# Kernel optimization log

Measured on AMD Instinct MI355X. Metric: run time of the kernel, lower is better.

Reference implementation:

```python
import jax, jax.numpy as jnp
import numpy as np

N, E, B_GRAPHS = 50000, 512000, 64
XD, ED, C, H, L = 16, 8, 64, 2, 2
EPS = 1e-5


def setup_inputs() -> dict:
    key = jax.random.key(0)
    ks = jax.random.split(key, 20)
    w = lambda k, shape: jax.random.normal(k, shape, jnp.float32) * 0.1
    return {
        "x": jax.random.normal(ks[0], (N, XD), jnp.float32),
        "edge_attr": jax.random.normal(ks[1], (E, ED), jnp.float32),
        "edge_src": jax.random.randint(ks[2], (E,), 0, N, dtype=jnp.int32),
        "edge_dst": jax.random.randint(ks[3], (E,), 0, N, dtype=jnp.int32),
        "batch": jnp.sort(jax.random.randint(ks[4], (N,), 0, B_GRAPHS, dtype=jnp.int32)),
        "node_W": w(ks[5], (XD, C)), "node_b": jnp.zeros((C,), jnp.float32),
        "edge_W": w(ks[6], (ED, C)), "edge_b": jnp.zeros((C,), jnp.float32),
        "Wq": w(ks[7], (L, C, H * C)), "bq": jnp.zeros((L, H * C), jnp.float32),
        "Wk": w(ks[8], (L, C, H * C)), "bk": jnp.zeros((L, H * C), jnp.float32),
        "Wv": w(ks[9], (L, C, H * C)), "bv": jnp.zeros((L, H * C), jnp.float32),
        "We": w(ks[10], (L, C, H * C)), "be": jnp.zeros((L, H * C), jnp.float32),
        "Wskip": w(ks[11], (L, C, C)), "bskip": jnp.zeros((L, C), jnp.float32),
        "gamma": jnp.ones((L, C), jnp.float32), "beta": jnp.zeros((L, C), jnp.float32),
        "gate_W": w(ks[12], (C, 1)), "gate_b": jnp.zeros((1,), jnp.float32),
        "out_W": w(ks[13], (C, 1)), "out_b": jnp.zeros((1,), jnp.float32),
    }


def reference(x, edge_attr, edge_src, edge_dst, batch,
              node_W, node_b, edge_W, edge_b,
              Wq, bq, Wk, bk, Wv, bv, We, be,
              Wskip, bskip, gamma, beta,
              gate_W, gate_b, out_W, out_b):
    n = x.shape[0]
    h = x @ node_W + node_b                       # node encoder: [N, C]
    e = edge_attr @ edge_W + edge_b               # edge encoder: [E, C]
    scale = 1.0 / jnp.sqrt(jnp.float32(C))
    for i in range(L):
        identity = h
        # TransformerConv (UniMP), concat=False -> mean over heads
        q = (h @ Wq[i] + bq[i]).reshape(n, H, C)
        k = (h @ Wk[i] + bk[i]).reshape(n, H, C)
        v = (h @ Wv[i] + bv[i]).reshape(n, H, C)
        ep = (e @ We[i] + be[i]).reshape(-1, H, C)
        k_e = k[edge_src] + ep                    # [E, H, C]
        v_e = v[edge_src] + ep                    # [E, H, C]
        logits = jnp.einsum('ehc,ehc->eh', q[edge_dst], k_e) * scale
        # segment softmax over incoming edges of each target node
        m = jax.ops.segment_max(logits, edge_dst, num_segments=n)
        a = jnp.exp(logits - m[edge_dst])
        denom = jax.ops.segment_sum(a, edge_dst, num_segments=n)
        alpha = a / denom[edge_dst]               # [E, H]
        agg = jax.ops.segment_sum(alpha[:, :, None] * v_e, edge_dst, num_segments=n)
        out = agg.mean(axis=1) + h @ Wskip[i] + bskip[i]   # root/skip term
        # BatchNorm1d (training mode, biased variance)
        mu = out.mean(axis=0)
        var = out.var(axis=0)
        out = gamma[i] * (out - mu) * jax.lax.rsqrt(var + EPS) + beta[i]
        out = jax.nn.leaky_relu(out, 0.01)
        h = out + identity                        # residual
    # GlobalAttention pooling over graphs
    gate = (h @ gate_W + gate_b)[:, 0]            # [N]
    gm = jax.ops.segment_max(gate, batch, num_segments=B_GRAPHS)
    ge = jnp.exp(gate - gm[batch])
    gd = jax.ops.segment_sum(ge, batch, num_segments=B_GRAPHS)
    wts = ge / gd[batch]
    pooled = jax.ops.segment_sum(wts[:, None] * h, batch, num_segments=B_GRAPHS)
    return jax.nn.sigmoid(pooled @ out_W + out_b)  # [B_GRAPHS, 1]
```

## Files before the change

### kernel.cpp

```cpp
#include <hip/hip_runtime.h>
#include <hip/hip_bf16.h>

typedef unsigned short ushort_t;
typedef __attribute__((ext_vector_type(8))) short short8;
typedef __attribute__((ext_vector_type(4))) float float4v;

__device__ __forceinline__ float bfu_lo(unsigned u) {
    return __uint_as_float(u << 16);
}
__device__ __forceinline__ float bfu_hi(unsigned u) {
    return __uint_as_float(u & 0xffff0000u);
}
__device__ __forceinline__ ushort_t f2bf(float f) {
    __hip_bfloat16 h = __float2bfloat16(f);
    return *reinterpret_cast<ushort_t*>(&h);
}



__global__ __launch_bounds__(256) void setup_kernel(
    const float* __restrict__ x, const float* __restrict__ node_W,
    const float* __restrict__ node_b,
    const float* __restrict__ edge_W, const float* __restrict__ edge_b,
    const float* __restrict__ We, const float* __restrict__ be,
    const float* __restrict__ Wq, const float* __restrict__ bq,
    const float* __restrict__ Wk, const float* __restrict__ bk,
    const float* __restrict__ Wv, const float* __restrict__ bv,
    const float* __restrict__ Wskip, const float* __restrict__ bskip,
    float* __restrict__ h, ushort_t* __restrict__ h_bf,
    int* __restrict__ counts,
    float* __restrict__ Wc, float* __restrict__ bcb,
    ushort_t* __restrict__ Wall_arr, float* __restrict__ Wall_bias,
    ushort_t* __restrict__ wv_arr,
    int O0, int O1, int O2, int N) {
    int b = blockIdx.x, t = threadIdx.x;
    if (b < O0) {
        int idx = b * 256 + t;
        if (idx < N * 64) {
            int n = idx >> 6, c = idx & 63;
            float acc = node_b[c];
#pragma unroll
            for (int j = 0; j < 16; ++j) acc += x[n * 16 + j] * node_W[j * 64 + c];
            h[idx] = acc;
            h_bf[idx] = f2bf(acc);
        }
    } else if (b < O1) {
        int i = (b - O0) * 256 + t;
        if (i < N) counts[i] = 0;
    } else if (b < O2) {
        int tid = (b - O1) * 256 + t;
        if (tid < 2048) {
            int l = tid >> 10, d = (tid >> 7) & 7, j = tid & 127;
            float s = 0.f;
            for (int m = 0; m < 64; ++m) s += edge_W[d * 64 + m] * We[l * 8192 + m * 128 + j];
            Wc[l * 1024 + d * 128 + j] = s;
        } else if (tid < 2048 + 256) {
            int u = tid - 2048;
            int l = u >> 7, j = u & 127;
            float s = be[l * 128 + j];
            for (int m = 0; m < 64; ++m) s += edge_b[m] * We[l * 8192 + m * 128 + j];
            bcb[l * 128 + j] = s;
        }
    } else {
        int tid = (b - O2) * 256 + t;
        if (tid < 2 * 14336) {
            int l = tid / 14336, u = tid % 14336;
            int j = u & 7, ln = (u >> 3) & 63, kch = (u >> 9) & 1, ct = u >> 10;
            int nn = ln & 15, quad = ln >> 4;
            int k = kch * 32 + quad * 8 + j;
            int col = ct * 16 + nn;
            float v = 0.f;
            if (col < 128) {
                int hh = col >> 6, m = col & 63;
                const float* wq = Wq + l * 8192 + k * 128 + hh * 64;
                const float* wk = Wk + l * 8192 + m * 128 + hh * 64;
                float s = 0.f;
                for (int c2 = 0; c2 < 64; ++c2) s += wq[c2] * wk[c2];
                v = 0.125f * s;
            } else if (col < 192) {
                v = Wskip[l * 4096 + k * 64 + (col - 128)];
            }
            Wall_arr[(size_t)l * 14336 + ct * 1024 + kch * 512 + ln * 8 + j] = f2bf(v);
        } else if (tid < 2 * 14336 + 2 * 224) {
            int u = tid - 2 * 14336;
            int l = u / 224, col = u % 224;
            float v = 0.f;
            if (col < 128) {
                int hh = col >> 6, m = col & 63;
                const float* bqp = bq + l * 128 + hh * 64;
                const float* wk = Wk + l * 8192 + m * 128 + hh * 64;
                float s = 0.f;
                for (int c2 = 0; c2 < 64; ++c2) s += bqp[c2] * wk[c2];
                v = 0.125f * s;
            } else if (col < 192) {
                v = bskip[l * 64 + col - 128];
            }
            Wall_bias[l * 224 + col] = v;
        } else if (tid < 2 * 14336 + 2 * 224 + 2 * 8192) {
            int u = tid - (2 * 14336 + 2 * 224);
            int l = u >> 13, r = u & 8191;
            int j = r & 7, ln = (r >> 3) & 63, ct = (r >> 9) & 3, kc = r >> 11;
            int quad = ln >> 4, nn = ln & 15;
            int p = kc * 32 + quad * 8 + j;
            int hh = p >> 6, m = p & 63;
            int c2 = ct * 16 + nn;
            wv_arr[(size_t)l * 8192 + r] = f2bf(Wv[l * 8192 + m * 128 + hh * 64 + c2]);
        }
    }
}

__global__ void combine2_kernel(const float* __restrict__ Wq, const float* __restrict__ bq,
                                const float* __restrict__ bk, const float* __restrict__ bv,
                                const float* __restrict__ Wc, const float* __restrict__ bcb,
                                ushort_t* __restrict__ Wall_arr, float* __restrict__ Wall_bias,
                                float* __restrict__ cst) {
    int tid = blockIdx.x * 256 + threadIdx.x;
    if (tid < 2304) {
        int l = tid / 1152, u = tid % 1152, k = u / 18, j = u % 18;
        float s = 0.f;
        if (j < 16) {
            int hh = j >> 3, d = j & 7;
            for (int c = 0; c < 64; ++c)
                s += Wq[l * 8192 + k * 128 + hh * 64 + c] * Wc[l * 1024 + d * 128 + hh * 64 + c];
        } else {
            int hh = j - 16;
            for (int c = 0; c < 64; ++c)
                s += Wq[l * 8192 + k * 128 + hh * 64 + c] *
                     (bcb[l * 128 + hh * 64 + c] + bk[l * 128 + hh * 64 + c]);
        }
        s *= 0.125f;
        int col = 192 + j;
        int ct = col >> 4, nn = col & 15;
        int kch = k >> 5, quad = (k >> 3) & 3, jj = k & 7;
        int ln = quad * 16 + nn;
        Wall_arr[(size_t)l * 14336 + ct * 1024 + kch * 512 + ln * 8 + jj] = f2bf(s);
    } else if (tid < 2304 + 36) {
        int u = tid - 2304;
        int l = u / 18, j = u % 18;
        float s = 0.f;
        if (j < 16) {
            int hh = j >> 3, d = j & 7;
            for (int c = 0; c < 64; ++c)
                s += bq[l * 128 + hh * 64 + c] * Wc[l * 1024 + d * 128 + hh * 64 + c];
        } else {
            int hh = j - 16;
            for (int c = 0; c < 64; ++c)
                s += bq[l * 128 + hh * 64 + c] *
                     (bcb[l * 128 + hh * 64 + c] + bk[l * 128 + hh * 64 + c]);
        }
        Wall_bias[l * 224 + 192 + j] = 0.125f * s;
    } else if (tid < 2304 + 36 + 128) {
        int u = tid - 2340;
        int l = u >> 6, c = u & 63;
        cst[l * 64 + c] = 0.5f * (bv[l * 128 + c] + bv[l * 128 + 64 + c] +
                                  bcb[l * 128 + c] + bcb[l * 128 + 64 + c]);
    }
}


__global__ void csr_count_kernel(const int* __restrict__ dst, int* __restrict__ counts, int E) {
    int e = blockIdx.x * 256 + threadIdx.x;
    if (e < E) atomicAdd(&counts[dst[e]], 1);
}

__global__ void scan1_kernel(const int* __restrict__ counts, int* __restrict__ rowptr,
                             int* __restrict__ bsums, int N) {
    __shared__ int s[256];
    int t = threadIdx.x, i = blockIdx.x * 256 + t;
    int v = (i < N) ? counts[i] : 0;
    s[t] = v;
    __syncthreads();
    for (int d = 1; d < 256; d <<= 1) {
        int x = (t >= d) ? s[t - d] : 0;
        __syncthreads();
        s[t] += x;
        __syncthreads();
    }
    if (i < N) rowptr[i] = s[t] - v;
    if (t == 255) bsums[blockIdx.x] = s[255];
}

__global__ void scan3_kernel(int* __restrict__ rowptr, const int* __restrict__ bsums,
                             int* __restrict__ cursor, int N, int E, int nb) {
    __shared__ int sh[256];
    int t = threadIdx.x;
    int v = (t < nb) ? bsums[t] : 0;
    sh[t] = v;
    __syncthreads();
    for (int d = 1; d < 256; d <<= 1) {
        int x = (t >= d) ? sh[t - d] : 0;
        __syncthreads();
        sh[t] += x;
        __syncthreads();
    }
    int blk = blockIdx.x;
    int offv = (blk == 0) ? 0 : sh[blk - 1];
    int i = blk * 256 + t;
    if (i < N) {
        int r = rowptr[i] + offv;
        rowptr[i] = r;
        cursor[i] = r;
    }
    if (i == 0) rowptr[N] = E;
}

__global__ void csr_fill_kernel(const int* __restrict__ dst, const int* __restrict__ src,
                                const float* __restrict__ edge_attr, int* __restrict__ cursor,
                                char* __restrict__ erec, int E) {
    int e = blockIdx.x * 256 + threadIdx.x;
    if (e < E) {
        int pos = atomicAdd(&cursor[dst[e]], 1);
        float4 a0 = *(const float4*)(edge_attr + (size_t)e * 8);
        float4 a1 = *(const float4*)(edge_attr + (size_t)e * 8 + 4);
        uint4 w1;
        w1.x = (unsigned)f2bf(a0.x) | ((unsigned)f2bf(a0.y) << 16);
        w1.y = (unsigned)f2bf(a0.z) | ((unsigned)f2bf(a0.w) << 16);
        w1.z = (unsigned)f2bf(a1.x) | ((unsigned)f2bf(a1.y) << 16);
        w1.w = (unsigned)f2bf(a1.z) | ((unsigned)f2bf(a1.w) << 16);
        char* rp = erec + (size_t)pos * 32;
        *(uint4*)rp = make_uint4((unsigned)(src[e] * 128), 0u, 0u, 0u);
        *(uint4*)(rp + 16) = w1;
    }
}


__device__ __forceinline__ void gemm_store(
    int col, float bias, float4v c, int nbase, int N,
    ushort_t* __restrict__ qk2buf, float* __restrict__ outbuf, float* __restrict__ qcbuf) {
    if (col < 128) {
        ushort_t* qp = qk2buf + (size_t)nbase * 128 + col;
#pragma unroll
        for (int r = 0; r < 4; ++r)
            if (nbase + r < N) qp[(size_t)r * 128] = f2bf(c[r] + bias);
    } else if (col < 192) {
        float* op = outbuf + (size_t)nbase * 64 + (col - 128);
#pragma unroll
        for (int r = 0; r < 4; ++r)
            if (nbase + r < N) op[(size_t)r * 64] = c[r] + bias;
    } else if (col < 210) {
        float* qp2 = qcbuf + (size_t)nbase * 20 + (col - 192);
#pragma unroll
        for (int r = 0; r < 4; ++r)
            if (nbase + r < N) qp2[(size_t)r * 20] = c[r] + bias;
    }
}

__global__ __launch_bounds__(256) void qkv_mfma_kernel(
    const ushort_t* __restrict__ h_bf,
    const ushort_t* __restrict__ Wall_arr, const float* __restrict__ Wall_bias,
    ushort_t* __restrict__ qk2buf, float* __restrict__ outbuf, float* __restrict__ qcbuf,
    int N) {
    int wave = threadIdx.x >> 6, lane = threadIdx.x & 63;
    int quad = lane >> 4, nn = lane & 15;
    int n0 = blockIdx.x * 32;
    int nodeA = n0 + nn;       if (nodeA >= N) nodeA = N - 1;
    int nodeB = n0 + 16 + nn;  if (nodeB >= N) nodeB = N - 1;
    const ushort_t* apA = h_bf + (size_t)nodeA * 64 + quad * 8;
    const ushort_t* apB = h_bf + (size_t)nodeB * 64 + quad * 8;
    short8 aA0 = *(const short8*)apA;
    short8 aA1 = *(const short8*)(apA + 32);
    short8 aB0 = *(const short8*)apB;
    short8 aB1 = *(const short8*)(apB + 32);
    int ct_start = (wave < 2) ? wave * 4 : (8 + (wave - 2) * 3);
    int ct_cnt = (wave < 2) ? 4 : 3;
    for (int i = 0; i < ct_cnt; ++i) {
        int ct = ct_start + i;
        const ushort_t* bp = Wall_arr + (size_t)ct * 1024 + lane * 8;
        short8 b0 = *(const short8*)bp;
        short8 b1 = *(const short8*)(bp + 512);
        float4v cA = {0.f, 0.f, 0.f, 0.f};
        float4v cB = {0.f, 0.f, 0.f, 0.f};
        cA = __builtin_amdgcn_mfma_f32_16x16x32_bf16(aA0, b0, cA, 0, 0, 0);
        cA = __builtin_amdgcn_mfma_f32_16x16x32_bf16(aA1, b1, cA, 0, 0, 0);
        cB = __builtin_amdgcn_mfma_f32_16x16x32_bf16(aB0, b0, cB, 0, 0, 0);
        cB = __builtin_amdgcn_mfma_f32_16x16x32_bf16(aB1, b1, cB, 0, 0, 0);
        int col = ct * 16 + nn;
        float bias = Wall_bias[col];
        gemm_store(col, bias, cA, n0 + quad * 4, N, qk2buf, outbuf, qcbuf);
        gemm_store(col, bias, cB, n0 + 16 + quad * 4, N, qk2buf, outbuf, qcbuf);
    }
}


__global__ __launch_bounds__(256) void bnqkv_kernel(
    const float* __restrict__ outbuf_in, const float* __restrict__ bnsums,
    const float* __restrict__ gamma, const float* __restrict__ beta,
    float* __restrict__ h, ushort_t* __restrict__ h_bf,
    const ushort_t* __restrict__ Wall_arr, const float* __restrict__ Wall_bias,
    ushort_t* __restrict__ qk2buf, float* __restrict__ outbuf, float* __restrict__ qcbuf,
    int N) {
    __shared__ ushort_t hb[32 * 64];
    __shared__ float ss_scale[64], ss_shift[64];
    int t = threadIdx.x;
    if (t < 64) {
        float invN = 1.f / (float)N;
        float mean = bnsums[t] * invN;
        float var = bnsums[64 + t] * invN - mean * mean;
        float sc = gamma[t] * rsqrtf(var + 1e-5f);
        ss_scale[t] = sc;
        ss_shift[t] = beta[t] - mean * sc;
    }
    __syncthreads();
    int n0 = blockIdx.x * 32;
    int c = t & 63;
    float sc = ss_scale[c], sh = ss_shift[c];
#pragma unroll
    for (int i = 0; i < 8; ++i) {
        int li = t + i * 256;
        int gidx = n0 * 64 + li;
        float hn = 0.f;
        if (gidx < N * 64) {
            float o = outbuf_in[gidx] * sc + sh;
            o = (o > 0.f) ? o : 0.01f * o;
            hn = h[gidx] + o;
            h[gidx] = hn;
            h_bf[gidx] = f2bf(hn);
        }
        hb[li] = f2bf(hn);
    }
    __syncthreads();
    int wave = t >> 6, lane = t & 63;
    int quad = lane >> 4, nn = lane & 15;
    const ushort_t* apA = hb + nn * 64 + quad * 8;
    const ushort_t* apB = hb + (16 + nn) * 64 + quad * 8;
    short8 aA0 = *(const short8*)apA;
    short8 aA1 = *(const short8*)(apA + 32);
    short8 aB0 = *(const short8*)apB;
    short8 aB1 = *(const short8*)(apB + 32);
    int ct_start = (wave < 2) ? wave * 4 : (8 + (wave - 2) * 3);
    int ct_cnt = (wave < 2) ? 4 : 3;
    for (int i = 0; i < ct_cnt; ++i) {
        int ct = ct_start + i;
        const ushort_t* bp = Wall_arr + (size_t)ct * 1024 + lane * 8;
        short8 b0 = *(const short8*)bp;
        short8 b1 = *(const short8*)(bp + 512);
        float4v cA = {0.f, 0.f, 0.f, 0.f};
        float4v cB = {0.f, 0.f, 0.f, 0.f};
        cA = __builtin_amdgcn_mfma_f32_16x16x32_bf16(aA0, b0, cA, 0, 0, 0);
        cA = __builtin_amdgcn_mfma_f32_16x16x32_bf16(aA1, b1, cA, 0, 0, 0);
        cB = __builtin_amdgcn_mfma_f32_16x16x32_bf16(aB0, b0, cB, 0, 0, 0);
        cB = __builtin_amdgcn_mfma_f32_16x16x32_bf16(aB1, b1, cB, 0, 0, 0);
        int col = ct * 16 + nn;
        float bias = Wall_bias[col];
        gemm_store(col, bias, cA, n0 + quad * 4, N, qk2buf, outbuf, qcbuf);
        gemm_store(col, bias, cB, n0 + 16 + quad * 4, N, qk2buf, outbuf, qcbuf);
    }
}


__global__ __launch_bounds__(256) void attn_kernel(
    const ushort_t* __restrict__ h_bf, const ushort_t* __restrict__ qk2buf,
    const float* __restrict__ qcbuf,
    const char* __restrict__ erec, const int* __restrict__ rowptr,
    ushort_t* __restrict__ haccn, float* __restrict__ sen, float* __restrict__ degw,
    int N) {
    int t = threadIdx.x;
    int lane = t & 63, wid = t >> 6;
    int grp = lane >> 4, l16 = lane & 15;
    int head = l16 >> 3, l8 = l16 & 7;
    const char* hbb = (const char*)h_bf;

    int n = blockIdx.x * 16 + wid * 4 + grp;
    bool active = (n < N);
    int nn = active ? n : (N - 1);
    int start = rowptr[nn];
    int deg = active ? (rowptr[nn + 1] - start) : 0;
    int wdeg = deg;
    wdeg = max(wdeg, __shfl_xor(wdeg, 16));
    wdeg = max(wdeg, __shfl_xor(wdeg, 32));

    float lsum = 0.f;
    float hacc[8] = {0.f, 0.f, 0.f, 0.f, 0.f, 0.f, 0.f, 0.f};
    float se[8]   = {0.f, 0.f, 0.f, 0.f, 0.f, 0.f, 0.f, 0.f};

    if (wdeg > 0) {
        uint4 qr = *(const uint4*)((const char*)qk2buf + (size_t)nn * 256 + head * 128 + l8 * 16);
        float qk0 = bfu_lo(qr.x), qk1 = bfu_hi(qr.x);
        float qk2f = bfu_lo(qr.y), qk3 = bfu_hi(qr.y);
        float qk4 = bfu_lo(qr.z), qk5 = bfu_hi(qr.z);
        float qk6 = bfu_lo(qr.w), qk7 = bfu_hi(qr.w);
        const float* qcp = qcbuf + (size_t)nn * 20;
        float4 qcA = *(const float4*)(qcp + head * 8);
        float4 qcB = *(const float4*)(qcp + head * 8 + 4);
        float qb = qcp[16 + head];

        bool dpos = (deg > 0);
        int dclamp = dpos ? (deg - 1) : 0;

        int offL = *(const int*)(erec + (size_t)(dpos ? (start + min(l16, dclamp)) : 0) * 32);
        int o0 = __shfl(offL, grp * 16);
        uint4 ca = *(const uint4*)(hbb + (size_t)(unsigned)o0 + l8 * 16);
        int gi0 = dpos ? start : 0;
        uint4 ev = *(const uint4*)(erec + (size_t)gi0 * 32 + 16);

        for (int it = 0; it < wdeg; ++it) {
            int itn = it + 1;
            if ((itn & 15) == 0)
                offL = *(const int*)(erec +
                        (size_t)(dpos ? (start + min(itn + l16, dclamp)) : 0) * 32);
            int itc = min(itn, wdeg - 1);
            int on = __shfl(offL, grp * 16 + (itc & 15));
            uint4 na = *(const uint4*)(hbb + (size_t)(unsigned)on + l8 * 16);
            int gin = dpos ? (start + min(itc, dclamp)) : 0;
            uint4 fv = *(const uint4*)(erec + (size_t)gin * 32 + 16);

            float h0 = bfu_lo(ca.x), h1 = bfu_hi(ca.x);
            float h2 = bfu_lo(ca.y), h3 = bfu_hi(ca.y);
            float h4 = bfu_lo(ca.z), h5 = bfu_hi(ca.z);
            float h6 = bfu_lo(ca.w), h7 = bfu_hi(ca.w);
            float dt = qk0 * h0 + qk1 * h1 + qk2f * h2 + qk3 * h3
                     + qk4 * h4 + qk5 * h5 + qk6 * h6 + qk7 * h7;
            dt += __shfl_xor(dt, 1);
            dt += __shfl_xor(dt, 2);
            dt += __shfl_xor(dt, 4);
            float ex0 = bfu_lo(ev.x), ex1 = bfu_hi(ev.x);
            float ex2 = bfu_lo(ev.y), ex3 = bfu_hi(ev.y);
            float ex4 = bfu_lo(ev.z), ex5 = bfu_hi(ev.z);
            float ex6 = bfu_lo(ev.w), ex7 = bfu_hi(ev.w);
            float s0 = dt
                     + qcA.x * ex0 + qcA.y * ex1 + qcA.z * ex2 + qcA.w * ex3
                     + qcB.x * ex4 + qcB.y * ex5 + qcB.z * ex6 + qcB.w * ex7
                     + qb;
            float p = (it < deg) ? __expf(fmaxf(s0, -60.f)) : 0.f;
            lsum += p;
            hacc[0] += p * h0; hacc[1] += p * h1;
            hacc[2] += p * h2; hacc[3] += p * h3;
            hacc[4] += p * h4; hacc[5] += p * h5;
            hacc[6] += p * h6; hacc[7] += p * h7;
            se[0] += p * ex0; se[1] += p * ex1; se[2] += p * ex2; se[3] += p * ex3;
            se[4] += p * ex4; se[5] += p * ex5; se[6] += p * ex6; se[7] += p * ex7;
            ca = na; ev = fv;
        }
    }

    if (active) {
        float inv = (deg > 0) ? (0.5f / lsum) : 0.f;
        unsigned pw0 = (unsigned)f2bf(hacc[0] * inv) | ((unsigned)f2bf(hacc[1] * inv) << 16);
        unsigned pw1 = (unsigned)f2bf(hacc[2] * inv) | ((unsigned)f2bf(hacc[3] * inv) << 16);
        unsigned pw2 = (unsigned)f2bf(hacc[4] * inv) | ((unsigned)f2bf(hacc[5] * inv) << 16);
        unsigned pw3 = (unsigned)f2bf(hacc[6] * inv) | ((unsigned)f2bf(hacc[7] * inv) << 16);
        uint4 pk = make_uint4(pw0, pw1, pw2, pw3);
        *(uint4*)((char*)haccn + (size_t)nn * 256 + head * 128 + l8 * 16) = pk;
        if (l8 == 0) {
            *(float4*)(sen + (size_t)nn * 16 + head * 8) =
                make_float4(se[0] * inv, se[1] * inv, se[2] * inv, se[3] * inv);
            *(float4*)(sen + (size_t)nn * 16 + head * 8 + 4) =
                make_float4(se[4] * inv, se[5] * inv, se[6] * inv, se[7] * inv);
            if (head == 0) degw[nn] = (deg > 0) ? 1.f : 0.f;
        }
    }
}


__global__ __launch_bounds__(256) void vapply_kernel(
    const ushort_t* __restrict__ haccn, const float* __restrict__ sen,
    const float* __restrict__ degw,
    const ushort_t* __restrict__ wv_arr, const float* __restrict__ Wc,
    const float* __restrict__ cst,
    float* __restrict__ outbuf, float* __restrict__ part, int N) {
    __shared__ float Wc_s[1024];
    __shared__ float cst_s[64];
    __shared__ float sen_s[32][16];
    __shared__ float dw_s[32];
    __shared__ float ps[128];
    int t = threadIdx.x;
    for (int i = t; i < 1024; i += 256) Wc_s[i] = Wc[i];
    if (t < 64) cst_s[t] = cst[t];
    int n0 = blockIdx.x * 32;
    for (int i = t; i < 512; i += 256) {
        int ln2 = i >> 4;
        int nc = n0 + ln2; if (nc >= N) nc = N - 1;
        sen_s[ln2][i & 15] = sen[(size_t)nc * 16 + (i & 15)];
    }
    if (t < 32) {
        int nc = n0 + t; if (nc >= N) nc = N - 1;
        dw_s[t] = degw[nc];
    }
    __syncthreads();
    int wave = t >> 6, lane = t & 63;
    int quad = lane >> 4, nn = lane & 15;
    int nodeA = n0 + nn;       if (nodeA >= N) nodeA = N - 1;
    int nodeB = n0 + 16 + nn;  if (nodeB >= N) nodeB = N - 1;
    int ct = wave;
    float4v cA = {0.f, 0.f, 0.f, 0.f};
    float4v cB = {0.f, 0.f, 0.f, 0.f};
#pragma unroll
    for (int kc = 0; kc < 4; ++kc) {
        short8 aA = *(const short8*)(haccn + (size_t)nodeA * 128 + kc * 32 + quad * 8);
        short8 aB = *(const short8*)(haccn + (size_t)nodeB * 128 + kc * 32 + quad * 8);
        short8 bb = *(const short8*)(wv_arr + kc * 2048 + ct * 512 + lane * 8);
        cA = __builtin_amdgcn_mfma_f32_16x16x32_bf16(aA, bb, cA, 0, 0, 0);
        cB = __builtin_amdgcn_mfma_f32_16x16x32_bf16(aB, bb, cB, 0, 0, 0);
    }
    int col = ct * 16 + nn;
    float sa = 0.f, sq = 0.f;
#pragma unroll
    for (int g = 0; g < 2; ++g) {
        float4v acc = g ? cB : cA;
        int lbase = g * 16 + quad * 4;
#pragma unroll
        for (int r = 0; r < 4; ++r) {
            int ln2 = lbase + r;
            int nr = n0 + ln2;
            const float* sp = sen_s[ln2];
            float ep = 0.f;
#pragma unroll
            for (int hh = 0; hh < 2; ++hh)
#pragma unroll
                for (int d = 0; d < 8; ++d)
                    ep += sp[hh * 8 + d] * Wc_s[d * 128 + hh * 64 + col];
            if (nr < N) {
                float val = acc[r] + ep + dw_s[ln2] * cst_s[col] +
                            outbuf[(size_t)nr * 64 + col];
                outbuf[(size_t)nr * 64 + col] = val;
                sa += val;
                sq += val * val;
            }
        }
    }
    sa += __shfl_xor(sa, 16); sa += __shfl_xor(sa, 32);
    sq += __shfl_xor(sq, 16); sq += __shfl_xor(sq, 32);
    if (quad == 0) { ps[col] = sa; ps[64 + col] = sq; }
    __syncthreads();
    if (t < 128) part[(size_t)blockIdx.x * 128 + t] = ps[t];
}


__global__ __launch_bounds__(256) void bnreduce_kernel(const float* __restrict__ part,
                                                       float* __restrict__ bnsums, int nb) {
    int s = blockIdx.x;
    int t = threadIdx.x;
    float a = 0.f;
    for (int b = t; b < nb; b += 256) a += part[(size_t)b * 128 + s];
    __shared__ float sh[256];
    sh[t] = a;
    __syncthreads();
    for (int d = 128; d; d >>= 1) {
        if (t < d) sh[t] += sh[t + d];
        __syncthreads();
    }
    if (t == 0) bnsums[s] = sh[0];
}

__global__ __launch_bounds__(256) void bnapply_kernel(
    const float* __restrict__ outbuf, const float* __restrict__ bnsums,
    const float* __restrict__ gamma, const float* __restrict__ beta,
    const float* __restrict__ gate_W, const float* __restrict__ gate_b,
    float* __restrict__ h, float* __restrict__ gatebuf, int N) {
    int idx = blockIdx.x * 256 + threadIdx.x;
    if (idx >= N * 64) return;
    int c = idx & 63, n = idx >> 6;
    float invN = 1.f / (float)N;
    float mean = bnsums[c] * invN;
    float var = bnsums[64 + c] * invN - mean * mean;
    float scale = gamma[c] * rsqrtf(var + 1e-5f);
    float shift = beta[c] - mean * scale;
    float o = outbuf[idx] * scale + shift;
    o = (o > 0.f) ? o : 0.01f * o;
    float hn = h[idx] + o;
    h[idx] = hn;
    float g = hn * gate_W[c];
#pragma unroll
    for (int off = 32; off; off >>= 1) g += __shfl_xor(g, off);
    if (c == 0) gatebuf[n] = g + gate_b[0];
}


__global__ __launch_bounds__(256) void pool_acc_kernel(
    const float* __restrict__ h, const float* __restrict__ gatebuf,
    const int* __restrict__ batch,
    float* __restrict__ pacc, float* __restrict__ pden, int N) {
    int b = blockIdx.x >> 3, chunk = blockIdx.x & 7;
    int lo = 0, hi = N;
    while (lo < hi) { int mid = (lo + hi) >> 1; if (batch[mid] < b) lo = mid + 1; else hi = mid; }
    int start = lo;
    lo = start; hi = N;
    while (lo < hi) { int mid = (lo + hi) >> 1; if (batch[mid] <= b) lo = mid + 1; else hi = mid; }
    int end = lo;
    int t = threadIdx.x, lane = t & 63, wid = t >> 6;
    __shared__ float sm[4];
    float mx = -1e30f;
    for (int n = start + t; n < end; n += 256) mx = fmaxf(mx, gatebuf[n]);
#pragma unroll
    for (int off = 32; off; off >>= 1) mx = fmaxf(mx, __shfl_xor(mx, off));
    if (lane == 0) sm[wid] = mx;
    __syncthreads();
    float mb = fmaxf(fmaxf(sm[0], sm[1]), fmaxf(sm[2], sm[3]));
    int gwid = chunk * 4 + wid;
    float acc = 0.f, den = 0.f;
    for (int n = start + gwid; n < end; n += 32) {
        float ge = __expf(gatebuf[n] - mb);
        acc += ge * h[(size_t)n * 64 + lane];
        den += ge;
    }
    __shared__ float sacc[4][64];
    __shared__ float sden[4];
    sacc[wid][lane] = acc;
    if (lane == 0) sden[wid] = den;
    __syncthreads();
    if (wid == 0) {
        pacc[(size_t)blockIdx.x * 64 + lane] =
            sacc[0][lane] + sacc[1][lane] + sacc[2][lane] + sacc[3][lane];
        if (lane == 0) pden[blockIdx.x] = sden[0] + sden[1] + sden[2] + sden[3];
    }
}

__global__ void pool_fin_kernel(const float* __restrict__ pacc, const float* __restrict__ pden,
                                const float* __restrict__ out_W, const float* __restrict__ out_b,
                                float* __restrict__ out) {
    int b = blockIdx.x, c = threadIdx.x;
    float pc = 0.f, dv = 0.f;
#pragma unroll
    for (int j = 0; j < 8; ++j) {
        pc += pacc[(size_t)(b * 8 + j) * 64 + c];
        dv += pden[b * 8 + j];
    }
    float s = pc * out_W[c];
#pragma unroll
    for (int off = 32; off; off >>= 1) s += __shfl_xor(s, off);
    if (c == 0) {
        if (dv <= 0.f) dv = 1.f;
        float v = s / dv + out_b[0];
        out[b] = 1.f / (1.f + __expf(-v));
    }
}


extern "C" void kernel_launch(void* const* d_in, const int* in_sizes, int n_in,
                              void* d_out, int out_size, void* d_ws, size_t ws_size,
                              hipStream_t stream) {
    const float* x         = (const float*)d_in[0];
    const float* edge_attr = (const float*)d_in[1];
    const int*   edge_src  = (const int*)d_in[2];
    const int*   edge_dst  = (const int*)d_in[3];
    const int*   batch     = (const int*)d_in[4];
    const float* node_W    = (const float*)d_in[5];
    const float* node_b    = (const float*)d_in[6];
    const float* edge_W    = (const float*)d_in[7];
    const float* edge_b    = (const float*)d_in[8];
    const float* Wq        = (const float*)d_in[9];
    const float* bq        = (const float*)d_in[10];
    const float* Wk        = (const float*)d_in[11];
    const float* bk        = (const float*)d_in[12];
    const float* Wv        = (const float*)d_in[13];
    const float* bv        = (const float*)d_in[14];
    const float* We        = (const float*)d_in[15];
    const float* be        = (const float*)d_in[16];
    const float* Wskip     = (const float*)d_in[17];
    const float* bskip     = (const float*)d_in[18];
    const float* gamma     = (const float*)d_in[19];
    const float* beta      = (const float*)d_in[20];
    const float* gate_W    = (const float*)d_in[21];
    const float* gate_b    = (const float*)d_in[22];
    const float* out_W     = (const float*)d_in[23];
    const float* out_b     = (const float*)d_in[24];
    float* out = (float*)d_out;

    const int N = in_sizes[0] / 16;
    const int E = in_sizes[2];
    const int nba = (N + 15) / 16;
    const int nbv = (N + 31) / 32;

    char* ws = (char*)d_ws;
    size_t off = 0;
    auto alloc = [&](size_t bytes) {
        size_t o = off;
        off += (bytes + 255) & ~(size_t)255;
        return o;
    };
    float*    h        = (float*)(ws + alloc((size_t)N * 64 * 4));
    ushort_t* h_bf     = (ushort_t*)(ws + alloc((size_t)N * 64 * 2));
    ushort_t* qk2buf   = (ushort_t*)(ws + alloc((size_t)N * 128 * 2));
    float*    outbuf   = (float*)(ws + alloc((size_t)N * 64 * 4));
    float*    qcbuf    = (float*)(ws + alloc((size_t)N * 20 * 4));
    ushort_t* haccn    = (ushort_t*)(ws + alloc((size_t)N * 128 * 2));
    float*    sen      = (float*)(ws + alloc((size_t)N * 16 * 4));
    float*    degw     = (float*)(ws + alloc((size_t)N * 4));
    int*      rowptr   = (int*)(ws + alloc((size_t)(N + 1) * 4));
    int*      cursor   = (int*)(ws + alloc((size_t)N * 4));
    int*      counts   = (int*)(ws + alloc((size_t)N * 4));
    int*      bsums    = (int*)(ws + alloc(1024));
    char*     erec     = (char*)(ws + alloc((size_t)E * 32));
    float*    Wc       = (float*)(ws + alloc(2 * 1024 * 4));
    float*    bcb      = (float*)(ws + alloc(2 * 128 * 4));
    ushort_t* Wall_arr = (ushort_t*)(ws + alloc(2 * 14336 * 2));
    float*    Wall_b   = (float*)(ws + alloc(2 * 224 * 4));
    ushort_t* wv_arr   = (ushort_t*)(ws + alloc(2 * 8192 * 2));
    float*    cst      = (float*)(ws + alloc(2 * 64 * 4));
    float*    bnsums   = (float*)(ws + alloc(128 * 4));
    float*    gatebuf  = (float*)(ws + alloc((size_t)N * 4));
    float*    part     = (float*)(ws + alloc((size_t)nbv * 128 * 4));
    float*    pacc     = (float*)(ws + alloc((size_t)512 * 64 * 4));
    float*    pden     = (float*)(ws + alloc(512 * 4));
    if (off > ws_size) return;

    int O0 = (N * 64 + 255) / 256;
    int O1 = O0 + (N + 255) / 256;
    int O2 = O1 + 9;
    int O3 = O2 + 178;
    setup_kernel<<<O3, 256, 0, stream>>>(
        x, node_W, node_b, edge_W, edge_b, We, be, Wq, bq, Wk, bk, Wv, bv, Wskip, bskip,
        h, h_bf, counts, Wc, bcb, Wall_arr, Wall_b, wv_arr, O0, O1, O2, N);
    combine2_kernel<<<10, 256, 0, stream>>>(Wq, bq, bk, bv, Wc, bcb, Wall_arr, Wall_b, cst);

    csr_count_kernel<<<(E + 255) / 256, 256, 0, stream>>>(edge_dst, counts, E);
    int nb = (N + 255) / 256;
    scan1_kernel<<<nb, 256, 0, stream>>>(counts, rowptr, bsums, N);
    scan3_kernel<<<nb, 256, 0, stream>>>(rowptr, bsums, cursor, N, E, nb);
    csr_fill_kernel<<<(E + 255) / 256, 256, 0, stream>>>(edge_dst, edge_src, edge_attr,
                                                         cursor, erec, E);

    qkv_mfma_kernel<<<nbv, 256, 0, stream>>>(
        h_bf, Wall_arr, Wall_b, qk2buf, outbuf, qcbuf, N);
    attn_kernel<<<nba, 256, 0, stream>>>(h_bf, qk2buf, qcbuf, erec,
                                         rowptr, haccn, sen, degw, N);
    vapply_kernel<<<nbv, 256, 0, stream>>>(haccn, sen, degw, wv_arr, Wc, cst,
                                           outbuf, part, N);
    bnreduce_kernel<<<128, 256, 0, stream>>>(part, bnsums, nbv);
    bnqkv_kernel<<<nbv, 256, 0, stream>>>(
        outbuf, bnsums, gamma, beta, h, h_bf,
        Wall_arr + 14336, Wall_b + 224, qk2buf, outbuf, qcbuf, N);

    attn_kernel<<<nba, 256, 0, stream>>>(h_bf, qk2buf, qcbuf, erec,
                                         rowptr, haccn, sen, degw, N);
    vapply_kernel<<<nbv, 256, 0, stream>>>(haccn, sen, degw, wv_arr + 8192, Wc + 1024,
                                           cst + 64, outbuf, part, N);
    bnreduce_kernel<<<128, 256, 0, stream>>>(part, bnsums, nbv);
    bnapply_kernel<<<(N * 64 + 255) / 256, 256, 0, stream>>>(
        outbuf, bnsums, gamma + 64, beta + 64, gate_W, gate_b, h, gatebuf, N);

    pool_acc_kernel<<<512, 256, 0, stream>>>(h, gatebuf, batch, pacc, pden, N);
    pool_fin_kernel<<<64, 64, 0, stream>>>(pacc, pden, out_W, out_b, out);
}
```

Baseline: 349.4 us.

## Fuse QKV projection, edge attention and value apply into one per-layer kernel

Merges the QKV MFMA projection, the per-node attention over incoming edges, and the value/skip projection with BN partial sums into a single 512-thread kernel per layer. The q/k, edge-coefficient, skip and aggregated results now live in shared memory instead of global buffers. To make this possible, the BN-apply step is split back out of the old fused bnqkv kernel into a separate elementwise kernel. This removes several global round trips and launches. In exchange it adds block-wide barriers between stages, so the irregular-degree attention phase can stall a whole block, and shared-memory use per block goes up, which may lower occupancy.

```diff
diff --git a/kernel.cpp b/kernel.cpp
--- a/kernel.cpp
+++ b/kernel.cpp
@@ -224,283 +224,171 @@
 }
 
 
-__device__ __forceinline__ void gemm_store(
-    int col, float bias, float4v c, int nbase, int N,
-    ushort_t* __restrict__ qk2buf, float* __restrict__ outbuf, float* __restrict__ qcbuf) {
-    if (col < 128) {
-        ushort_t* qp = qk2buf + (size_t)nbase * 128 + col;
-#pragma unroll
-        for (int r = 0; r < 4; ++r)
-            if (nbase + r < N) qp[(size_t)r * 128] = f2bf(c[r] + bias);
-    } else if (col < 192) {
-        float* op = outbuf + (size_t)nbase * 64 + (col - 128);
-#pragma unroll
-        for (int r = 0; r < 4; ++r)
-            if (nbase + r < N) op[(size_t)r * 64] = c[r] + bias;
-    } else if (col < 210) {
-        float* qp2 = qcbuf + (size_t)nbase * 20 + (col - 192);
-#pragma unroll
-        for (int r = 0; r < 4; ++r)
-            if (nbase + r < N) qp2[(size_t)r * 20] = c[r] + bias;
-    }
-}
-
-__global__ __launch_bounds__(256) void qkv_mfma_kernel(
+__global__ __launch_bounds__(512) void layer_kernel(
     const ushort_t* __restrict__ h_bf,
+    const char* __restrict__ erec, const int* __restrict__ rowptr,
     const ushort_t* __restrict__ Wall_arr, const float* __restrict__ Wall_bias,
-    ushort_t* __restrict__ qk2buf, float* __restrict__ outbuf, float* __restrict__ qcbuf,
-    int N) {
-    int wave = threadIdx.x >> 6, lane = threadIdx.x & 63;
-    int quad = lane >> 4, nn = lane & 15;
-    int n0 = blockIdx.x * 32;
-    int nodeA = n0 + nn;       if (nodeA >= N) nodeA = N - 1;
-    int nodeB = n0 + 16 + nn;  if (nodeB >= N) nodeB = N - 1;
-    const ushort_t* apA = h_bf + (size_t)nodeA * 64 + quad * 8;
-    const ushort_t* apB = h_bf + (size_t)nodeB * 64 + quad * 8;
-    short8 aA0 = *(const short8*)apA;
-    short8 aA1 = *(const short8*)(apA + 32);
-    short8 aB0 = *(const short8*)apB;
-    short8 aB1 = *(const short8*)(apB + 32);
-    int ct_start = (wave < 2) ? wave * 4 : (8 + (wave - 2) * 3);
-    int ct_cnt = (wave < 2) ? 4 : 3;
-    for (int i = 0; i < ct_cnt; ++i) {
-        int ct = ct_start + i;
-        const ushort_t* bp = Wall_arr + (size_t)ct * 1024 + lane * 8;
-        short8 b0 = *(const short8*)bp;
-        short8 b1 = *(const short8*)(bp + 512);
-        float4v cA = {0.f, 0.f, 0.f, 0.f};
-        float4v cB = {0.f, 0.f, 0.f, 0.f};
-        cA = __builtin_amdgcn_mfma_f32_16x16x32_bf16(aA0, b0, cA, 0, 0, 0);
-        cA = __builtin_amdgcn_mfma_f32_16x16x32_bf16(aA1, b1, cA, 0, 0, 0);
-        cB = __builtin_amdgcn_mfma_f32_16x16x32_bf16(aB0, b0, cB, 0, 0, 0);
-        cB = __builtin_amdgcn_mfma_f32_16x16x32_bf16(aB1, b1, cB, 0, 0, 0);
-        int col = ct * 16 + nn;
-        float bias = Wall_bias[col];
-        gemm_store(col, bias, cA, n0 + quad * 4, N, qk2buf, outbuf, qcbuf);
-        gemm_store(col, bias, cB, n0 + 16 + quad * 4, N, qk2buf, outbuf, qcbuf);
-    }
-}
-
-
-__global__ __launch_bounds__(256) void bnqkv_kernel(
-    const float* __restrict__ outbuf_in, const float* __restrict__ bnsums,
-    const float* __restrict__ gamma, const float* __restrict__ beta,
-    float* __restrict__ h, ushort_t* __restrict__ h_bf,
-    const ushort_t* __restrict__ Wall_arr, const float* __restrict__ Wall_bias,
-    ushort_t* __restrict__ qk2buf, float* __restrict__ outbuf, float* __restrict__ qcbuf,
-    int N) {
-    __shared__ ushort_t hb[32 * 64];
-    __shared__ float ss_scale[64], ss_shift[64];
-    int t = threadIdx.x;
-    if (t < 64) {
-        float invN = 1.f / (float)N;
-        float mean = bnsums[t] * invN;
-        float var = bnsums[64 + t] * invN - mean * mean;
-        float sc = gamma[t] * rsqrtf(var + 1e-5f);
-        ss_scale[t] = sc;
-        ss_shift[t] = beta[t] - mean * sc;
-    }
-    __syncthreads();
-    int n0 = blockIdx.x * 32;
-    int c = t & 63;
-    float sc = ss_scale[c], sh = ss_shift[c];
-#pragma unroll
-    for (int i = 0; i < 8; ++i) {
-        int li = t + i * 256;
-        int gidx = n0 * 64 + li;
-        float hn = 0.f;
-        if (gidx < N * 64) {
-            float o = outbuf_in[gidx] * sc + sh;
-            o = (o > 0.f) ? o : 0.01f * o;
-            hn = h[gidx] + o;
-            h[gidx] = hn;
-            h_bf[gidx] = f2bf(hn);
-        }
-        hb[li] = f2bf(hn);
-    }
-    __syncthreads();
-    int wave = t >> 6, lane = t & 63;
-    int quad = lane >> 4, nn = lane & 15;
-    const ushort_t* apA = hb + nn * 64 + quad * 8;
-    const ushort_t* apB = hb + (16 + nn) * 64 + quad * 8;
-    short8 aA0 = *(const short8*)apA;
-    short8 aA1 = *(const short8*)(apA + 32);
-    short8 aB0 = *(const short8*)apB;
-    short8 aB1 = *(const short8*)(apB + 32);
-    int ct_start = (wave < 2) ? wave * 4 : (8 + (wave - 2) * 3);
-    int ct_cnt = (wave < 2) ? 4 : 3;
-    for (int i = 0; i < ct_cnt; ++i) {
-        int ct = ct_start + i;
-        const ushort_t* bp = Wall_arr + (size_t)ct * 1024 + lane * 8;
-        short8 b0 = *(const short8*)bp;
-        short8 b1 = *(const short8*)(bp + 512);
-        float4v cA = {0.f, 0.f, 0.f, 0.f};
-        float4v cB = {0.f, 0.f, 0.f, 0.f};
-        cA = __builtin_amdgcn_mfma_f32_16x16x32_bf16(aA0, b0, cA, 0, 0, 0);
-        cA = __builtin_amdgcn_mfma_f32_16x16x32_bf16(aA1, b1, cA, 0, 0, 0);
-        cB = __builtin_amdgcn_mfma_f32_16x16x32_bf16(aB0, b0, cB, 0, 0, 0);
-        cB = __builtin_amdgcn_mfma_f32_16x16x32_bf16(aB1, b1, cB, 0, 0, 0);
-        int col = ct * 16 + nn;
-        float bias = Wall_bias[col];
-        gemm_store(col, bias, cA, n0 + quad * 4, N, qk2buf, outbuf, qcbuf);
-        gemm_store(col, bias, cB, n0 + 16 + quad * 4, N, qk2buf, outbuf, qcbuf);
-    }
-}
-
-
-__global__ __launch_bounds__(256) void attn_kernel(
-    const ushort_t* __restrict__ h_bf, const ushort_t* __restrict__ qk2buf,
-    const float* __restrict__ qcbuf,
-    const char* __restrict__ erec, const int* __restrict__ rowptr,
-    ushort_t* __restrict__ haccn, float* __restrict__ sen, float* __restrict__ degw,
-    int N) {
-    int t = threadIdx.x;
-    int lane = t & 63, wid = t >> 6;
-    int grp = lane >> 4, l16 = lane & 15;
-    int head = l16 >> 3, l8 = l16 & 7;
-    const char* hbb = (const char*)h_bf;
-
-    int n = blockIdx.x * 16 + wid * 4 + grp;
-    bool active = (n < N);
-    int nn = active ? n : (N - 1);
-    int start = rowptr[nn];
-    int deg = active ? (rowptr[nn + 1] - start) : 0;
-    int wdeg = deg;
-    wdeg = max(wdeg, __shfl_xor(wdeg, 16));
-    wdeg = max(wdeg, __shfl_xor(wdeg, 32));
-
-    float lsum = 0.f;
-    float hacc[8] = {0.f, 0.f, 0.f, 0.f, 0.f, 0.f, 0.f, 0.f};
-    float se[8]   = {0.f, 0.f, 0.f, 0.f, 0.f, 0.f, 0.f, 0.f};
-
-    if (wdeg > 0) {
-        uint4 qr = *(const uint4*)((const char*)qk2buf + (size_t)nn * 256 + head * 128 + l8 * 16);
-        float qk0 = bfu_lo(qr.x), qk1 = bfu_hi(qr.x);
-        float qk2f = bfu_lo(qr.y), qk3 = bfu_hi(qr.y);
-        float qk4 = bfu_lo(qr.z), qk5 = bfu_hi(qr.z);
-        float qk6 = bfu_lo(qr.w), qk7 = bfu_hi(qr.w);
-        const float* qcp = qcbuf + (size_t)nn * 20;
-        float4 qcA = *(const float4*)(qcp + head * 8);
-        float4 qcB = *(const float4*)(qcp + head * 8 + 4);
-        float qb = qcp[16 + head];
-
-        bool dpos = (deg > 0);
-        int dclamp = dpos ? (deg - 1) : 0;
-
-        int offL = *(const int*)(erec + (size_t)(dpos ? (start + min(l16, dclamp)) : 0) * 32);
-        int o0 = __shfl(offL, grp * 16);
-        uint4 ca = *(const uint4*)(hbb + (size_t)(unsigned)o0 + l8 * 16);
-        int gi0 = dpos ? start : 0;
-        uint4 ev = *(const uint4*)(erec + (size_t)gi0 * 32 + 16);
-
-        for (int it = 0; it < wdeg; ++it) {
-            int itn = it + 1;
-            if ((itn & 15) == 0)
-                offL = *(const int*)(erec +
-                        (size_t)(dpos ? (start + min(itn + l16, dclamp)) : 0) * 32);
-            int itc = min(itn, wdeg - 1);
-            int on = __shfl(offL, grp * 16 + (itc & 15));
-            uint4 na = *(const uint4*)(hbb + (size_t)(unsigned)on + l8 * 16);
-            int gin = dpos ? (start + min(itc, dclamp)) : 0;
-            uint4 fv = *(const uint4*)(erec + (size_t)gin * 32 + 16);
-
-            float h0 = bfu_lo(ca.x), h1 = bfu_hi(ca.x);
-            float h2 = bfu_lo(ca.y), h3 = bfu_hi(ca.y);
-            float h4 = bfu_lo(ca.z), h5 = bfu_hi(ca.z);
-            float h6 = bfu_lo(ca.w), h7 = bfu_hi(ca.w);
-            float dt = qk0 * h0 + qk1 * h1 + qk2f * h2 + qk3 * h3
-                     + qk4 * h4 + qk5 * h5 + qk6 * h6 + qk7 * h7;
-            dt += __shfl_xor(dt, 1);
-            dt += __shfl_xor(dt, 2);
-            dt += __shfl_xor(dt, 4);
-            float ex0 = bfu_lo(ev.x), ex1 = bfu_hi(ev.x);
-            float ex2 = bfu_lo(ev.y), ex3 = bfu_hi(ev.y);
-            float ex4 = bfu_lo(ev.z), ex5 = bfu_hi(ev.z);
-            float ex6 = bfu_lo(ev.w), ex7 = bfu_hi(ev.w);
-            float s0 = dt
-                     + qcA.x * ex0 + qcA.y * ex1 + qcA.z * ex2 + qcA.w * ex3
-                     + qcB.x * ex4 + qcB.y * ex5 + qcB.z * ex6 + qcB.w * ex7
-                     + qb;
-            float p = (it < deg) ? __expf(fmaxf(s0, -60.f)) : 0.f;
-            lsum += p;
-            hacc[0] += p * h0; hacc[1] += p * h1;
-            hacc[2] += p * h2; hacc[3] += p * h3;
-            hacc[4] += p * h4; hacc[5] += p * h5;
-            hacc[6] += p * h6; hacc[7] += p * h7;
-            se[0] += p * ex0; se[1] += p * ex1; se[2] += p * ex2; se[3] += p * ex3;
-            se[4] += p * ex4; se[5] += p * ex5; se[6] += p * ex6; se[7] += p * ex7;
-            ca = na; ev = fv;
-        }
-    }
-
-    if (active) {
-        float inv = (deg > 0) ? (0.5f / lsum) : 0.f;
-        unsigned pw0 = (unsigned)f2bf(hacc[0] * inv) | ((unsigned)f2bf(hacc[1] * inv) << 16);
-        unsigned pw1 = (unsigned)f2bf(hacc[2] * inv) | ((unsigned)f2bf(hacc[3] * inv) << 16);
-        unsigned pw2 = (unsigned)f2bf(hacc[4] * inv) | ((unsigned)f2bf(hacc[5] * inv) << 16);
-        unsigned pw3 = (unsigned)f2bf(hacc[6] * inv) | ((unsigned)f2bf(hacc[7] * inv) << 16);
-        uint4 pk = make_uint4(pw0, pw1, pw2, pw3);
-        *(uint4*)((char*)haccn + (size_t)nn * 256 + head * 128 + l8 * 16) = pk;
-        if (l8 == 0) {
-            *(float4*)(sen + (size_t)nn * 16 + head * 8) =
-                make_float4(se[0] * inv, se[1] * inv, se[2] * inv, se[3] * inv);
-            *(float4*)(sen + (size_t)nn * 16 + head * 8 + 4) =
-                make_float4(se[4] * inv, se[5] * inv, se[6] * inv, se[7] * inv);
-            if (head == 0) degw[nn] = (deg > 0) ? 1.f : 0.f;
-        }
-    }
-}
-
-
-__global__ __launch_bounds__(256) void vapply_kernel(
-    const ushort_t* __restrict__ haccn, const float* __restrict__ sen,
-    const float* __restrict__ degw,
     const ushort_t* __restrict__ wv_arr, const float* __restrict__ Wc,
     const float* __restrict__ cst,
     float* __restrict__ outbuf, float* __restrict__ part, int N) {
+    __shared__ ushort_t qk2_s[32][128];
+    __shared__ ushort_t ha_s[32][136];
+    __shared__ float qc_s[32][20];
+    __shared__ float skip_s[32][64];
+    __shared__ float sen_s[32][16];
+    __shared__ float dw_s[32];
     __shared__ float Wc_s[1024];
     __shared__ float cst_s[64];
-    __shared__ float sen_s[32][16];
-    __shared__ float dw_s[32];
-    __shared__ float ps[128];
+    __shared__ float ps[2][128];
     int t = threadIdx.x;
-    for (int i = t; i < 1024; i += 256) Wc_s[i] = Wc[i];
+    int lane = t & 63, wid = t >> 6;
+    int n0 = blockIdx.x * 32;
+    for (int i = t; i < 1024; i += 512) Wc_s[i] = Wc[i];
     if (t < 64) cst_s[t] = cst[t];
-    int n0 = blockIdx.x * 32;
-    for (int i = t; i < 512; i += 256) {
-        int ln2 = i >> 4;
-        int nc = n0 + ln2; if (nc >= N) nc = N - 1;
-        sen_s[ln2][i & 15] = sen[(size_t)nc * 16 + (i & 15)];
-    }
-    if (t < 32) {
-        int nc = n0 + t; if (nc >= N) nc = N - 1;
-        dw_s[t] = degw[nc];
-    }
-    __syncthreads();
-    int wave = t >> 6, lane = t & 63;
-    int quad = lane >> 4, nn = lane & 15;
-    int nodeA = n0 + nn;       if (nodeA >= N) nodeA = N - 1;
-    int nodeB = n0 + 16 + nn;  if (nodeB >= N) nodeB = N - 1;
-    int ct = wave;
-    float4v cA = {0.f, 0.f, 0.f, 0.f};
-    float4v cB = {0.f, 0.f, 0.f, 0.f};
-#pragma unroll
-    for (int kc = 0; kc < 4; ++kc) {
-        short8 aA = *(const short8*)(haccn + (size_t)nodeA * 128 + kc * 32 + quad * 8);
-        short8 aB = *(const short8*)(haccn + (size_t)nodeB * 128 + kc * 32 + quad * 8);
-        short8 bb = *(const short8*)(wv_arr + kc * 2048 + ct * 512 + lane * 8);
-        cA = __builtin_amdgcn_mfma_f32_16x16x32_bf16(aA, bb, cA, 0, 0, 0);
-        cB = __builtin_amdgcn_mfma_f32_16x16x32_bf16(aB, bb, cB, 0, 0, 0);
-    }
-    int col = ct * 16 + nn;
-    float sa = 0.f, sq = 0.f;
-#pragma unroll
-    for (int g = 0; g < 2; ++g) {
-        float4v acc = g ? cB : cA;
-        int lbase = g * 16 + quad * 4;
+
+    {
+        int quad = lane >> 4, nn16 = lane & 15;
+        int nodeA = n0 + nn16;      if (nodeA >= N) nodeA = N - 1;
+        int nodeB = n0 + 16 + nn16; if (nodeB >= N) nodeB = N - 1;
+        const ushort_t* apA = h_bf + (size_t)nodeA * 64 + quad * 8;
+        const ushort_t* apB = h_bf + (size_t)nodeB * 64 + quad * 8;
+        short8 aA0 = *(const short8*)apA;
+        short8 aA1 = *(const short8*)(apA + 32);
+        short8 aB0 = *(const short8*)apB;
+        short8 aB1 = *(const short8*)(apB + 32);
+        for (int ct = wid; ct < 14; ct += 8) {
+            const ushort_t* bp = Wall_arr + (size_t)ct * 1024 + lane * 8;
+            short8 b0 = *(const short8*)bp;
+            short8 b1 = *(const short8*)(bp + 512);
+            float4v cA = {0.f, 0.f, 0.f, 0.f};
+            float4v cB = {0.f, 0.f, 0.f, 0.f};
+            cA = __builtin_amdgcn_mfma_f32_16x16x32_bf16(aA0, b0, cA, 0, 0, 0);
+            cA = __builtin_amdgcn_mfma_f32_16x16x32_bf16(aA1, b1, cA, 0, 0, 0);
+            cB = __builtin_amdgcn_mfma_f32_16x16x32_bf16(aB0, b0, cB, 0, 0, 0);
+            cB = __builtin_amdgcn_mfma_f32_16x16x32_bf16(aB1, b1, cB, 0, 0, 0);
+            int col = ct * 16 + nn16;
+            float bias = Wall_bias[col];
+#pragma unroll
+            for (int g = 0; g < 2; ++g) {
+                float4v c = g ? cB : cA;
+                int lbase = g * 16 + quad * 4;
+#pragma unroll
+                for (int r = 0; r < 4; ++r) {
+                    float v = c[r] + bias;
+                    int ln2 = lbase + r;
+                    if (col < 128) qk2_s[ln2][col] = f2bf(v);
+                    else if (col < 192) skip_s[ln2][col - 128] = v;
+                    else if (col < 210) qc_s[ln2][col - 192] = v;
+                }
+            }
+        }
+    }
+    __syncthreads();
+
+    {
+        int grp = lane >> 4, l16 = lane & 15;
+        int head = l16 >> 3, l8 = l16 & 7;
+        const char* hbb = (const char*)h_bf;
+        int ln = wid * 4 + grp;
+        int n = n0 + ln;
+        bool active = (n < N);
+        int nn = active ? n : (N - 1);
+        int start = rowptr[nn];
+        int deg = active ? (rowptr[nn + 1] - start) : 0;
+        int wdeg = deg;
+        wdeg = max(wdeg, __shfl_xor(wdeg, 16));
+        wdeg = max(wdeg, __shfl_xor(wdeg, 32));
+
+        float lsum = 0.f;
+        float hacc[8] = {0.f, 0.f, 0.f, 0.f, 0.f, 0.f, 0.f, 0.f};
+        float se[8]   = {0.f, 0.f, 0.f, 0.f, 0.f, 0.f, 0.f, 0.f};
+
+        if (wdeg > 0) {
+            uint4 qr = *(const uint4*)&qk2_s[ln][head * 64 + l8 * 8];
+            float qk0 = bfu_lo(qr.x), qk1 = bfu_hi(qr.x);
+            float qk2f = bfu_lo(qr.y), qk3 = bfu_hi(qr.y);
+            float qk4 = bfu_lo(qr.z), qk5 = bfu_hi(qr.z);
+            float qk6 = bfu_lo(qr.w), qk7 = bfu_hi(qr.w);
+            float4 qcA = *(const float4*)&qc_s[ln][head * 8];
+            float4 qcB = *(const float4*)&qc_s[ln][head * 8 + 4];
+            float qb = qc_s[ln][16 + head];
+
+            bool dpos = (deg > 0);
+            int dclamp = dpos ? (deg - 1) : 0;
+
+            int offL = *(const int*)(erec + (size_t)(dpos ? (start + min(l16, dclamp)) : 0) * 32);
+            int o0 = __shfl(offL, grp * 16);
+            uint4 ca = *(const uint4*)(hbb + (size_t)(unsigned)o0 + l8 * 16);
+            int gi0 = dpos ? start : 0;
+            uint4 ev = *(const uint4*)(erec + (size_t)gi0 * 32 + 16);
+
+            for (int it = 0; it < wdeg; ++it) {
+                int itn = it + 1;
+                if ((itn & 15) == 0)
+                    offL = *(const int*)(erec +
+                            (size_t)(dpos ? (start + min(itn + l16, dclamp)) : 0) * 32);
+                int itc = min(itn, wdeg - 1);
+                int on = __shfl(offL, grp * 16 + (itc & 15));
+                uint4 na = *(const uint4*)(hbb + (size_t)(unsigned)on + l8 * 16);
+                int gin = dpos ? (start + min(itc, dclamp)) : 0;
+                uint4 fv = *(const uint4*)(erec + (size_t)gin * 32 + 16);
+
+                float h0 = bfu_lo(ca.x), h1 = bfu_hi(ca.x);
+                float h2 = bfu_lo(ca.y), h3 = bfu_hi(ca.y);
+                float h4 = bfu_lo(ca.z), h5 = bfu_hi(ca.z);
+                float h6 = bfu_lo(ca.w), h7 = bfu_hi(ca.w);
+                float dt = qk0 * h0 + qk1 * h1 + qk2f * h2 + qk3 * h3
+                         + qk4 * h4 + qk5 * h5 + qk6 * h6 + qk7 * h7;
+                dt += __shfl_xor(dt, 1);
+                dt += __shfl_xor(dt, 2);
+                dt += __shfl_xor(dt, 4);
+                float ex0 = bfu_lo(ev.x), ex1 = bfu_hi(ev.x);
+                float ex2 = bfu_lo(ev.y), ex3 = bfu_hi(ev.y);
+                float ex4 = bfu_lo(ev.z), ex5 = bfu_hi(ev.z);
+                float ex6 = bfu_lo(ev.w), ex7 = bfu_hi(ev.w);
+                float s0 = dt
+                         + qcA.x * ex0 + qcA.y * ex1 + qcA.z * ex2 + qcA.w * ex3
+                         + qcB.x * ex4 + qcB.y * ex5 + qcB.z * ex6 + qcB.w * ex7
+                         + qb;
+                float p = (it < deg) ? __expf(fmaxf(s0, -60.f)) : 0.f;
+                lsum += p;
+                hacc[0] += p * h0; hacc[1] += p * h1;
+                hacc[2] += p * h2; hacc[3] += p * h3;
+                hacc[4] += p * h4; hacc[5] += p * h5;
+                hacc[6] += p * h6; hacc[7] += p * h7;
+                se[0] += p * ex0; se[1] += p * ex1; se[2] += p * ex2; se[3] += p * ex3;
+                se[4] += p * ex4; se[5] += p * ex5; se[6] += p * ex6; se[7] += p * ex7;
+                ca = na; ev = fv;
+            }
+        }
+
+        float inv = (deg > 0) ? (0.5f / lsum) : 0.f;
+#pragma unroll
+        for (int j2 = 0; j2 < 8; ++j2)
+            ha_s[ln][head * 64 + l8 * 8 + j2] = f2bf(hacc[j2] * inv);
+        if (l8 == 0) {
+#pragma unroll
+            for (int m = 0; m < 8; ++m) sen_s[ln][head * 8 + m] = se[m] * inv;
+            if (head == 0) dw_s[ln] = (deg > 0) ? 1.f : 0.f;
+        }
+    }
+    __syncthreads();
+
+    {
+        int quad = lane >> 4, nn16 = lane & 15;
+        int ct = wid & 3, g = wid >> 2;
+        float4v c = {0.f, 0.f, 0.f, 0.f};
+#pragma unroll
+        for (int kc = 0; kc < 4; ++kc) {
+            short8 a = *(const short8*)&ha_s[g * 16 + nn16][kc * 32 + quad * 8];
+            short8 b = *(const short8*)(wv_arr + kc * 2048 + ct * 512 + lane * 8);
+            c = __builtin_amdgcn_mfma_f32_16x16x32_bf16(a, b, c, 0, 0, 0);
+        }
+        int col = ct * 16 + nn16;
+        float sa = 0.f, sq = 0.f;
 #pragma unroll
         for (int r = 0; r < 4; ++r) {
-            int ln2 = lbase + r;
+            int ln2 = g * 16 + quad * 4 + r;
             int nr = n0 + ln2;
             const float* sp = sen_s[ln2];
             float ep = 0.f;
@@ -510,19 +398,18 @@
                 for (int d = 0; d < 8; ++d)
                     ep += sp[hh * 8 + d] * Wc_s[d * 128 + hh * 64 + col];
             if (nr < N) {
-                float val = acc[r] + ep + dw_s[ln2] * cst_s[col] +
-                            outbuf[(size_t)nr * 64 + col];
+                float val = c[r] + ep + dw_s[ln2] * cst_s[col] + skip_s[ln2][col];
                 outbuf[(size_t)nr * 64 + col] = val;
                 sa += val;
                 sq += val * val;
             }
         }
-    }
-    sa += __shfl_xor(sa, 16); sa += __shfl_xor(sa, 32);
-    sq += __shfl_xor(sq, 16); sq += __shfl_xor(sq, 32);
-    if (quad == 0) { ps[col] = sa; ps[64 + col] = sq; }
-    __syncthreads();
-    if (t < 128) part[(size_t)blockIdx.x * 128 + t] = ps[t];
+        sa += __shfl_xor(sa, 16); sa += __shfl_xor(sa, 32);
+        sq += __shfl_xor(sq, 16); sq += __shfl_xor(sq, 32);
+        if (quad == 0) { ps[g][col] = sa; ps[g][64 + col] = sq; }
+    }
+    __syncthreads();
+    if (t < 128) part[(size_t)blockIdx.x * 128 + t] = ps[0][t] + ps[1][t];
 }
 
 
@@ -540,6 +427,25 @@
         __syncthreads();
     }
     if (t == 0) bnsums[s] = sh[0];
+}
+
+__global__ __launch_bounds__(256) void bnh_kernel(
+    const float* __restrict__ outbuf, const float* __restrict__ bnsums,
+    const float* __restrict__ gamma, const float* __restrict__ beta,
+    float* __restrict__ h, ushort_t* __restrict__ h_bf, int N) {
+    int idx = blockIdx.x * 256 + threadIdx.x;
+    if (idx >= N * 64) return;
+    int c = idx & 63;
+    float invN = 1.f / (float)N;
+    float mean = bnsums[c] * invN;
+    float var = bnsums[64 + c] * invN - mean * mean;
+    float scale = gamma[c] * rsqrtf(var + 1e-5f);
+    float shift = beta[c] - mean * scale;
+    float o = outbuf[idx] * scale + shift;
+    o = (o > 0.f) ? o : 0.01f * o;
+    float hn = h[idx] + o;
+    h[idx] = hn;
+    h_bf[idx] = f2bf(hn);
 }
 
 __global__ __launch_bounds__(256) void bnapply_kernel(
@@ -658,7 +564,6 @@
 
     const int N = in_sizes[0] / 16;
     const int E = in_sizes[2];
-    const int nba = (N + 15) / 16;
     const int nbv = (N + 31) / 32;
 
     char* ws = (char*)d_ws;
@@ -670,12 +575,7 @@
     };
     float*    h        = (float*)(ws + alloc((size_t)N * 64 * 4));
     ushort_t* h_bf     = (ushort_t*)(ws + alloc((size_t)N * 64 * 2));
-    ushort_t* qk2buf   = (ushort_t*)(ws + alloc((size_t)N * 128 * 2));
     float*    outbuf   = (float*)(ws + alloc((size_t)N * 64 * 4));
-    float*    qcbuf    = (float*)(ws + alloc((size_t)N * 20 * 4));
-    ushort_t* haccn    = (ushort_t*)(ws + alloc((size_t)N * 128 * 2));
-    float*    sen      = (float*)(ws + alloc((size_t)N * 16 * 4));
-    float*    degw     = (float*)(ws + alloc((size_t)N * 4));
     int*      rowptr   = (int*)(ws + alloc((size_t)(N + 1) * 4));
     int*      cursor   = (int*)(ws + alloc((size_t)N * 4));
     int*      counts   = (int*)(ws + alloc((size_t)N * 4));
@@ -710,21 +610,17 @@
     csr_fill_kernel<<<(E + 255) / 256, 256, 0, stream>>>(edge_dst, edge_src, edge_attr,
                                                          cursor, erec, E);
 
-    qkv_mfma_kernel<<<nbv, 256, 0, stream>>>(
-        h_bf, Wall_arr, Wall_b, qk2buf, outbuf, qcbuf, N);
-    attn_kernel<<<nba, 256, 0, stream>>>(h_bf, qk2buf, qcbuf, erec,
-                                         rowptr, haccn, sen, degw, N);
-    vapply_kernel<<<nbv, 256, 0, stream>>>(haccn, sen, degw, wv_arr, Wc, cst,
-                                           outbuf, part, N);
+    layer_kernel<<<nbv, 512, 0, stream>>>(h_bf, erec, rowptr,
+                                          Wall_arr, Wall_b, wv_arr, Wc, cst,
+                                          outbuf, part, N);
     bnreduce_kernel<<<128, 256, 0, stream>>>(part, bnsums, nbv);
-    bnqkv_kernel<<<nbv, 256, 0, stream>>>(
-        outbuf, bnsums, gamma, beta, h, h_bf,
-        Wall_arr + 14336, Wall_b + 224, qk2buf, outbuf, qcbuf, N);
-
-    attn_kernel<<<nba, 256, 0, stream>>>(h_bf, qk2buf, qcbuf, erec,
-                                         rowptr, haccn, sen, degw, N);
-    vapply_kernel<<<nbv, 256, 0, stream>>>(haccn, sen, degw, wv_arr + 8192, Wc + 1024,
-                                           cst + 64, outbuf, part, N);
+    bnh_kernel<<<(N * 64 + 255) / 256, 256, 0, stream>>>(
+        outbuf, bnsums, gamma, beta, h, h_bf, N);
+
+    layer_kernel<<<nbv, 512, 0, stream>>>(h_bf, erec, rowptr,
+                                          Wall_arr + 14336, Wall_b + 224, wv_arr + 8192,
+                                          Wc + 1024, cst + 64,
+                                          outbuf, part, N);
     bnreduce_kernel<<<128, 256, 0, stream>>>(part, bnsums, nbv);
     bnapply_kernel<<<(N * 64 + 255) / 256, 256, 0, stream>>>(
         outbuf, bnsums, gamma + 64, beta + 64, gate_W, gate_b, h, gatebuf, N);
```

Measured after the change: 341.5 us. 1.02x faster.
